# Optimization experiments

Measured on AMD Instinct MI355X. Metric: run time of the kernel, lower is better.

Reference implementation:

```python
import jax, jax.numpy as jnp
import numpy as np

EMO = 1024
FEAT = 1024
K = 128  # aggregation_k
H_LIST = (4, 8, 16)
D_LIST = tuple(EMO // h for h in H_LIST)  # (256, 128, 64)
D_SUM = sum(D_LIST)  # 448
H_SUM = sum(H_LIST)  # 28
N = len(H_LIST)      # 3 subspaces
TEMP = float(np.power(D_SUM, 0.5))


def _block_mask(sizes, total):
    m = np.zeros((len(sizes), total), np.float32)
    off = 0
    for i, s in enumerate(sizes):
        m[i, off:off + s] = 1.0
        off += s
    return jnp.asarray(m)

M_Q_BLK = _block_mask(D_LIST, D_SUM)  # [N, d_sum]
M_V_BLK = _block_mask(H_LIST, H_SUM)  # [N, h_sum]


def setup_inputs() -> dict:
    key = jax.random.key(0)
    ks = iter(jax.random.split(key, 32))
    nrm = lambda shape, s=1.0: jax.random.normal(next(ks), shape, jnp.float32) * s
    B, Lt, Lp, Nv = 32, 1024, 512, 256
    return {
        "emo_embedding": nrm((B, Lt, EMO)),
        "phr_feat": nrm((B, Lp, FEAT)),
        "video_feat": nrm((B, Nv, FEAT)),
        "w_v_W": nrm((FEAT, FEAT), FEAT ** -0.5), "w_v_b": nrm((FEAT,), 0.01),
        "agg_a_W": nrm((FEAT, K), FEAT ** -0.5), "agg_a_b": nrm((K,), 0.01),
        "agg_c_W": nrm((FEAT, EMO), FEAT ** -0.5), "agg_c_b": nrm((EMO,), 0.01),
        "ele_W": nrm((2 * EMO, 1), (2 * EMO) ** -0.5), "ele_b": nrm((1,), 0.01),
        "wq_W": nrm((EMO, D_SUM), EMO ** -0.5), "wq_b": nrm((D_SUM,), 0.01),
        "wk_W": nrm((EMO, D_SUM), EMO ** -0.5), "wk_b": nrm((D_SUM,), 0.01),
        "wv_W": nrm((EMO, H_SUM), EMO ** -0.5), "wv_b": nrm((H_SUM,), 0.01),
        "wr_W": nrm((EMO, N), EMO ** -0.5), "wr_b": nrm((N,), 0.01),
    }


def reference(emo_embedding, phr_feat, video_feat,
              w_v_W, w_v_b, agg_a_W, agg_a_b, agg_c_W, agg_c_b,
              ele_W, ele_b, wq_W, wq_b, wk_W, wk_b, wv_W, wv_b, wr_W, wr_b):
    B, Lt, _ = emo_embedding.shape
    Nv = video_feat.shape[1]
    Lp = phr_feat.shape[1]

    # --- feature_aggregation ---
    # AdaptiveAvgPool1d(Nv); Lp % Nv == 0 so it is an exact reshape-mean.
    phr = phr_feat.reshape(B, Nv, Lp // Nv, FEAT).mean(axis=2)
    combine = jnp.concatenate([phr @ w_v_W + w_v_b, video_feat], axis=1)   # [B, 2*Nv, FEAT]
    attn_a = jax.nn.softmax(combine @ agg_a_W + agg_a_b, axis=-1)          # [B, 2*Nv, K]
    agg_feat = jnp.einsum('bmk,bme->bke', attn_a, combine @ agg_c_W + agg_c_b)  # [B, K, EMO]

    # --- element_routing ---
    A_pool = jnp.einsum('ble,bke->blk', emo_embedding, agg_feat).mean(axis=1)   # [B, K]
    route = jnp.einsum('bk,bke->be', A_pool, agg_feat)[:, None, :]              # [B, 1, EMO]
    route = jnp.broadcast_to(route, emo_embedding.shape)
    R_e = jnp.tanh(jnp.concatenate([emo_embedding, route], axis=-1) @ ele_W + ele_b)  # [B, Lt, 1]
    route_emo = R_e * emo_embedding                                              # [B, Lt, EMO]

    # --- subspace_routing ---
    Q = route_emo @ wq_W + wq_b        # [B, Lt, d_sum]
    Kp = agg_feat @ wk_W + wk_b        # [B, K, d_sum]
    V = agg_feat @ wv_W + wv_b         # [B, K, h_sum]
    Rp = agg_feat @ wr_W + wr_b        # [B, K, N]

    # N masked copies of Q (block subspace masks); K/R are plain repeats, V is masked.
    Qm = (Q[:, None] * M_Q_BLK[None, :, None, :]).reshape(B, N * Lt, D_SUM)
    Kf = jnp.tile(Kp, (1, N, 1))                                         # [B, N*K, d_sum]
    Vf = (V[:, None] * M_V_BLK[None, :, None, :]).reshape(B, N * K, H_SUM)
    Rf = jnp.tile(Rp, (1, N, 1))                                         # [B, N*K, N]

    attn = jax.nn.softmax(jnp.einsum('bqd,bkd->bqk', Qm, Kf) / TEMP, axis=-1)  # [B, N*Lt, N*K]
    O = jnp.tanh(attn @ Vf).reshape(B, N, Lt, H_SUM)
    O_R = (attn @ Rf).reshape(B, N, Lt, N)

    # per-subspace head gating of route_emo
    T_list = []
    hoff = 0
    for i in range(N):
        hi, di = H_LIST[i], D_LIST[i]
        ori = route_emo.reshape(B, Lt, hi, di)
        Oi = O[:, i, :, hoff:hoff + hi][..., None]      # [B, Lt, hi, 1]
        T_list.append((ori * Oi).reshape(B, Lt, EMO))
        hoff += hi
    T = jnp.stack(T_list, axis=1)                        # [B, N, Lt, EMO]

    Rdiag = jnp.stack([O_R[:, j, :, j].mean(axis=-1) for j in range(N)], axis=1)  # [B, N]
    gate = jax.nn.softmax(Rdiag, axis=-1)[:, :, None, None]
    return emo_embedding + (gate * T).sum(axis=1)
```

## Files before the change

### kernel.cpp

```cpp
#include <hip/hip_runtime.h>
#include <math.h>

typedef long long i64;
typedef __attribute__((ext_vector_type(8))) short bf16x8;
typedef __attribute__((ext_vector_type(4))) float f32x4;

#define TEMP_ISQ 0.047245559f

__device__ __forceinline__ unsigned short f2b(float x) {
  union { float f; unsigned u; } a; a.f = x;
  return (unsigned short)((a.u + 0x7fffu + ((a.u >> 16) & 1u)) >> 16);
}
__device__ __forceinline__ float b2f(unsigned short b) {
  union { float f; unsigned u; } a; a.u = ((unsigned)b) << 16; return a.f;
}

template<int BIAS, int OUTM, int RS, int BZDIV, int XMODE = 0>
__global__ __launch_bounds__(256)
void gemm_mfma(const unsigned short* __restrict__ Ab, i64 sA,
               const unsigned short* __restrict__ Bb, i64 sB,
               const float* __restrict__ bias,
               void* __restrict__ Ob, i64 sO,
               unsigned short* __restrict__ O2b, i64 sO2,
               int Nn, int Kd, int ldA, int ldB, int ldO,
               const float* __restrict__ rowScale, i64 sRS,
               const float* __restrict__ rsAdd)
{
  __shared__ unsigned short As[2][4096];
  __shared__ unsigned short Bs[2][4096];
  const int tid = threadIdx.x;
  const int w = tid >> 6, lane = tid & 63;

  const int gx = gridDim.x, gy = gridDim.y;
  int nwg = gx * gy * gridDim.z;
  int bid = blockIdx.x + gx * (blockIdx.y + gy * blockIdx.z);
  int L = bid;
  if ((nwg & 7) == 0) L = (bid & 7) * (nwg >> 3) + (bid >> 3);
  const int bx = L % gx;
  int rem = L / gx;
  const int by = rem % gy;
  const int z  = rem / gy;

  const int m0 = by * 128, n0 = bx * 128;
  const unsigned short* A;
  const unsigned short* B;
  int KdL = Kd;
  if (XMODE == 1) {
    int bb = z / 3, ii = z - bb * 3;
    const int dof_[3] = {0, 256, 384};
    const int kdt_[3] = {256, 128, 64};
    A = Ab + dof_[ii] + (i64)bb * sA;
    B = Bb + dof_[ii] + (i64)bb * sB;
    KdL = kdt_[ii];
  } else {
    A = Ab + (i64)z * sA;
    B = Bb + (i64)(BZDIV == 1 ? z : z / BZDIV) * sB;
  }
  const int wr = w >> 1, wc = w & 1;
  const int rS = tid >> 2, sS = tid & 3;
  const int cL = lane & 15, sl = lane >> 4;

  f32x4 acc[4][4];
  #pragma unroll
  for (int i = 0; i < 4; ++i)
    #pragma unroll
    for (int j = 0; j < 4; ++j) acc[i][j] = (f32x4){0.f, 0.f, 0.f, 0.f};

  auto STAGE = [&](int buf, int k0) {
    #pragma unroll
    for (int q = 0; q < 2; ++q) {
      int r = rS + q * 64;
      int sg = sS ^ (r & 3);
      const unsigned short* sa = A + (i64)(m0 + r) * ldA + k0 + sg * 8;
      const unsigned short* sb = B + (i64)(n0 + r) * ldB + k0 + sg * 8;
      __builtin_amdgcn_global_load_lds(
          (__attribute__((address_space(1))) void*)sa,
          (__attribute__((address_space(3))) void*)&As[buf][r * 32 + sS * 8], 16, 0, 0);
      __builtin_amdgcn_global_load_lds(
          (__attribute__((address_space(1))) void*)sb,
          (__attribute__((address_space(3))) void*)&Bs[buf][r * 32 + sS * 8], 16, 0, 0);
    }
  };

  STAGE(0, 0);
  __syncthreads();

  for (int k0 = 0; k0 < KdL; k0 += 32) {
    const int cur = (k0 >> 5) & 1;
    if (k0 + 32 < KdL) STAGE(cur ^ 1, k0 + 32);
    bf16x8 af[4], bfv[4];
    #pragma unroll
    for (int mi = 0; mi < 4; ++mi) {
      int rr = wr * 64 + mi * 16 + cL;
      int ph = sl ^ (rr & 3);
      af[mi] = *(const bf16x8*)&As[cur][rr * 32 + ph * 8];
    }
    #pragma unroll
    for (int ni = 0; ni < 4; ++ni) {
      int rr = wc * 64 + ni * 16 + cL;
      int ph = sl ^ (rr & 3);
      bfv[ni] = *(const bf16x8*)&Bs[cur][rr * 32 + ph * 8];
    }
    #pragma unroll
    for (int mi = 0; mi < 4; ++mi)
      #pragma unroll
      for (int ni = 0; ni < 4; ++ni)
        acc[mi][ni] = __builtin_amdgcn_mfma_f32_16x16x32_bf16(af[mi], bfv[ni], acc[mi][ni], 0, 0, 0);
    __syncthreads();
  }

  #pragma unroll
  for (int mi = 0; mi < 4; ++mi) {
    const int rowb = m0 + wr * 64 + mi * 16 + sl * 4;
    #pragma unroll
    for (int ni = 0; ni < 4; ++ni) {
      const int col = n0 + wc * 64 + ni * 16 + cL;
      if (col < Nn) {
        float bc = (BIAS == 1) ? bias[col] : 0.f;
        #pragma unroll
        for (int rg = 0; rg < 4; ++rg) {
          float v = acc[mi][ni][rg];
          if (RS) v *= tanhf(rowScale[(i64)z * sRS + rowb + rg] + rsAdd[z]);
          v += bc;
          if (BIAS == 2) v += bias[rowb + rg];
          i64 oidx = (i64)(rowb + rg) * ldO + col;
          if (OUTM == 0)      ((float*)Ob)[(i64)z * sO + oidx] = v;
          else if (OUTM == 1) ((unsigned short*)Ob)[(i64)z * sO + oidx] = f2b(v);
          else if (OUTM == 3) ((float*)Ob)[(i64)z * sO + oidx] = tanhf(v * (1.f / 3.f));
          else {
            ((float*)Ob)[(i64)z * sO + oidx] = v;
            O2b[(i64)z * sO2 + oidx] = f2b(v);
          }
        }
      }
    }
  }
}

__global__ __launch_bounds__(256)
void emo_pass1(const float* __restrict__ emo, const float* __restrict__ eleW,
               unsigned short* __restrict__ emoB, float* __restrict__ colPart,
               float* __restrict__ dotE) {
  int b = blockIdx.y, lc = blockIdx.x;
  int t = threadIdx.x, lane = t & 63, w = t >> 6;
  float4 w4 = ((const float4*)eleW)[t];
  float4 acc = make_float4(0.f, 0.f, 0.f, 0.f);
  __shared__ float dw[16][4];
  const float4* src = (const float4*)emo + ((i64)b * 1024 + lc * 16) * 256;
  ushort4* dst = (ushort4*)emoB + ((i64)b * 1024 + lc * 16) * 256;
  #pragma unroll 4
  for (int lr = 0; lr < 16; ++lr) {
    float4 v = src[lr * 256 + t];
    acc.x += v.x; acc.y += v.y; acc.z += v.z; acc.w += v.w;
    float d = v.x * w4.x + v.y * w4.y + v.z * w4.z + v.w * w4.w;
    #pragma unroll
    for (int o = 32; o; o >>= 1) d += __shfl_xor(d, o);
    if (!lane) dw[lr][w] = d;
    ushort4 o4; o4.x = f2b(v.x); o4.y = f2b(v.y); o4.z = f2b(v.z); o4.w = f2b(v.w);
    dst[lr * 256 + t] = o4;
  }
  __syncthreads();
  if (t < 16) dotE[(i64)b * 1024 + lc * 16 + t] = dw[t][0] + dw[t][1] + dw[t][2] + dw[t][3];
  ((float4*)colPart)[((i64)b * 64 + lc) * 256 + t] = acc;
}

__global__ void colmean2(const float* __restrict__ colPart, float* __restrict__ emomean) {
  int b = blockIdx.y, e = blockIdx.x * 256 + threadIdx.x;
  float s = 0.f;
  #pragma unroll 8
  for (int lc = 0; lc < 64; ++lc) s += colPart[((i64)b * 64 + lc) * 1024 + e];
  emomean[b * 1024 + e] = s * (1.f / 1024.f);
}

__global__ __launch_bounds__(256)
void transpose_all(const float* __restrict__ w_v_W, const float* __restrict__ agg_a_W,
                   const float* __restrict__ agg_c_W, const float* __restrict__ wq_W,
                   const float* __restrict__ wk_W, const float* __restrict__ wv_W,
                   const float* __restrict__ wr_W,
                   unsigned short* __restrict__ wvT, unsigned short* __restrict__ aaT,
                   unsigned short* __restrict__ acT, unsigned short* __restrict__ wqT,
                   unsigned short* __restrict__ kvrT) {
  __shared__ float T[32][33];
  int bx = blockIdx.x;
  const float* in; unsigned short* out; int N, Npad, s0;
  if (bx < 32)      { in = w_v_W;   out = wvT;                     N = 1024; Npad = 1024; s0 = 0; }
  else if (bx < 36) { in = agg_a_W; out = aaT;                     N = 128;  Npad = 128;  s0 = 32; }
  else if (bx < 68) { in = agg_c_W; out = acT;                     N = 1024; Npad = 1024; s0 = 36; }
  else if (bx < 84) { in = wq_W;    out = wqT;                     N = 448;  Npad = 512;  s0 = 68; }
  else if (bx < 98) { in = wk_W;    out = kvrT;                    N = 448;  Npad = 448;  s0 = 84; }
  else if (bx < 99) { in = wv_W;    out = kvrT + (i64)448 * 1024;  N = 28;   Npad = 28;   s0 = 98; }
  else              { in = wr_W;    out = kvrT + (i64)476 * 1024;  N = 3;    Npad = 36;   s0 = 99; }
  int n0 = (bx - s0) * 32, k0 = blockIdx.y * 32;
  int t = threadIdx.x;
  #pragma unroll
  for (int p = 0; p < 4; ++p) {
    int idx = t + 256 * p; int kk = idx >> 5, nn = idx & 31;
    float v = 0.f;
    if (n0 + nn < N) v = in[(i64)(k0 + kk) * N + (n0 + nn)];
    T[nn][kk] = v;
  }
  __syncthreads();
  #pragma unroll
  for (int p = 0; p < 4; ++p) {
    int idx = t + 256 * p; int nn = idx >> 5, kk = idx & 31;
    if (n0 + nn < Npad) out[(i64)(n0 + nn) * 1024 + (k0 + kk)] = f2b(T[nn][kk]);
  }
}

__global__ void kvr_bias_kernel(const float* wkb, const float* wvb, const float* wrb, float* out) {
  int t = blockIdx.x * 256 + threadIdx.x;
  if (t >= 480) return;
  out[t] = (t < 448) ? wkb[t] : (t < 476) ? wvb[t - 448] : (t < 479) ? wrb[t - 476] : 0.f;
}

__global__ void pool_phr(const float* __restrict__ phr, unsigned short* __restrict__ out) {
  i64 idx = (i64)blockIdx.x * 256 + threadIdx.x;
  if (idx >= 2097152) return;
  i64 bm = idx >> 8; int c = (int)(idx & 255);
  i64 b = bm >> 8, m = bm & 255;
  const float4* r0 = (const float4*)(phr + (b * 512 + 2 * m) * 1024) + c;
  const float4* r1 = (const float4*)(phr + (b * 512 + 2 * m + 1) * 1024) + c;
  float4 a = *r0, d = *r1;
  ushort4 o;
  o.x = f2b(0.5f * (a.x + d.x)); o.y = f2b(0.5f * (a.y + d.y));
  o.z = f2b(0.5f * (a.z + d.z)); o.w = f2b(0.5f * (a.w + d.w));
  ((ushort4*)out)[idx] = o;
}

__global__ void vconv(const float* __restrict__ video, unsigned short* __restrict__ combine) {
  i64 idx = (i64)blockIdx.x * 256 + threadIdx.x;
  if (idx >= 2097152) return;
  i64 b = idx >> 16, r = idx & 65535;
  float4 v = ((const float4*)video)[idx];
  ushort4 o;
  o.x = f2b(v.x); o.y = f2b(v.y); o.z = f2b(v.z); o.w = f2b(v.w);
  ((ushort4*)combine)[b * 131072 + 65536 + r] = o;
}

__global__ void vt_fill(const unsigned short* __restrict__ KVR, unsigned short* __restrict__ VT) {
  int b = blockIdx.y;
  int idx = blockIdx.x * 256 + threadIdx.x;
  int n = idx >> 7, k = idx & 127;
  unsigned short v = 0;
  if (n < 28) v = KVR[(i64)b * 61440 + k * 480 + 448 + n];
  VT[((i64)b * 128 + n) * 128 + k] = v;
}

__global__ void softmax_attn_a(const float* __restrict__ logits, unsigned short* __restrict__ outT) {
  int gw = (int)(((i64)blockIdx.x * blockDim.x + threadIdx.x) >> 6);
  int lane = threadIdx.x & 63;
  if (gw >= 32 * 512) return;
  int b = gw >> 9, m = gw & 511;
  const float* p = logits + (i64)gw * 128;
  float x0 = p[lane], x1 = p[lane + 64];
  float mx = fmaxf(x0, x1);
  #pragma unroll
  for (int o = 32; o; o >>= 1) mx = fmaxf(mx, __shfl_xor(mx, o));
  float e0 = expf(x0 - mx), e1 = expf(x1 - mx);
  float s = e0 + e1;
  #pragma unroll
  for (int o = 32; o; o >>= 1) s += __shfl_xor(s, o);
  float inv = 1.f / s;
  unsigned short* o0 = outT + (i64)b * 128 * 512 + m;
  o0[(i64)lane * 512] = f2b(e0 * inv);
  o0[(i64)(lane + 64) * 512] = f2b(e1 * inv);
}

__global__ void softmax_P_bf(const unsigned short* __restrict__ PL, unsigned short* __restrict__ P) {
  i64 gw = ((i64)blockIdx.x * blockDim.x + threadIdx.x) >> 6;
  int lane = threadIdx.x & 63;
  if (gw >= 98304) return;
  const unsigned short* p = PL + gw * 128;
  float x0 = b2f(p[lane]) * TEMP_ISQ, x1 = b2f(p[lane + 64]) * TEMP_ISQ;
  float mx = fmaxf(x0, x1);
  #pragma unroll
  for (int o = 32; o; o >>= 1) mx = fmaxf(mx, __shfl_xor(mx, o));
  float e0 = expf(x0 - mx), e1 = expf(x1 - mx);
  float s = e0 + e1;
  #pragma unroll
  for (int o = 32; o; o >>= 1) s += __shfl_xor(s, o);
  float inv = 1.f / s;
  P[gw * 128 + lane] = f2b(e0 * inv);
  P[gw * 128 + lane + 64] = f2b(e1 * inv);
}

__global__ void apool_kernel(const float* __restrict__ emomean, const float* __restrict__ agg,
                             float* __restrict__ Apool) {
  int gw = (int)(((i64)blockIdx.x * blockDim.x + threadIdx.x) >> 6);
  int lane = threadIdx.x & 63;
  if (gw >= 32 * 128) return;
  int b = gw >> 7, k = gw & 127;
  const float* ag = agg + ((i64)b * 128 + k) * 1024;
  const float* em = emomean + (i64)b * 1024;
  float s = 0.f;
  #pragma unroll
  for (int j = 0; j < 16; ++j) { int e = j * 64 + lane; s += em[e] * ag[e]; }
  #pragma unroll
  for (int o = 32; o; o >>= 1) s += __shfl_down(s, o);
  if (!lane) Apool[gw] = s;
}

__global__ void route_kernel(const float* __restrict__ Apool, const float* __restrict__ agg,
                             float* __restrict__ route) {
  int b = blockIdx.y;
  int e = blockIdx.x * 256 + threadIdx.x;
  __shared__ float Ap[128];
  if (threadIdx.x < 128) Ap[threadIdx.x] = Apool[b * 128 + threadIdx.x];
  __syncthreads();
  const float* ag = agg + (i64)b * 128 * 1024 + e;
  float s = 0.f;
  #pragma unroll 8
  for (int k = 0; k < 128; ++k) s += Ap[k] * ag[(i64)k * 1024];
  route[b * 1024 + e] = s;
}

__global__ void rb_kernel(const float* __restrict__ route, const float* __restrict__ eleW,
                          const float* __restrict__ eleb, float* __restrict__ rb) {
  int b = blockIdx.x, t = threadIdx.x;
  float s = 0.f;
  for (int j = t; j < 1024; j += 256) s += route[b * 1024 + j] * eleW[1024 + j];
  __shared__ float red[256];
  red[t] = s; __syncthreads();
  for (int o = 128; o > 0; o >>= 1) { if (t < o) red[t] += red[t + o]; __syncthreads(); }
  if (t == 0) rb[b] = red[0] + eleb[0];
}

__global__ void pmean1_kernel(const unsigned short* __restrict__ P, float* __restrict__ Ppart) {
  int bi = blockIdx.x, c = blockIdx.y, k = threadIdx.x;
  const unsigned short* p = P + ((i64)bi * 1024 + c * 128) * 128 + k;
  float s = 0.f;
  for (int l = 0; l < 128; ++l) s += b2f(p[(i64)l * 128]);
  Ppart[((i64)bi * 8 + c) * 128 + k] = s;
}

__global__ void pmean2_rdiag(const float* __restrict__ Ppart, const unsigned short* __restrict__ KVR,
                             float* __restrict__ gate) {
  int b = blockIdx.x, t = threadIdx.x;
  __shared__ float red[128];
  __shared__ float rd[3];
  for (int i = 0; i < 3; ++i) {
    float s = 0.f;
    #pragma unroll
    for (int c = 0; c < 8; ++c) s += Ppart[((i64)(b * 3 + i) * 8 + c) * 128 + t];
    float v = s * (1.f / 1024.f) * b2f(KVR[(i64)b * 61440 + t * 480 + 476 + i]);
    red[t] = v; __syncthreads();
    for (int o = 64; o > 0; o >>= 1) { if (t < o) red[t] += red[t + o]; __syncthreads(); }
    if (t == 0) rd[i] = red[0];
    __syncthreads();
  }
  if (t == 0) {
    float m = fmaxf(rd[0], fmaxf(rd[1], rd[2]));
    float e0 = expf(rd[0] - m), e1 = expf(rd[1] - m), e2 = expf(rd[2] - m);
    float inv = 1.f / (e0 + e1 + e2);
    gate[b * 3 + 0] = e0 * inv; gate[b * 3 + 1] = e1 * inv; gate[b * 3 + 2] = e2 * inv;
  }
}

__global__ __launch_bounds__(256)
void final_kernel(const unsigned short* __restrict__ emoB, const float* __restrict__ dotE,
                  const float* __restrict__ rbv, const float* __restrict__ O,
                  const float* __restrict__ gate, float* __restrict__ out) {
  i64 bl = blockIdx.x;
  int b = (int)(bl >> 10), l = (int)(bl & 1023);
  __shared__ float Gg[16];
  int t = threadIdx.x;
  if (t < 16) {
    float g0 = gate[b * 3], g1 = gate[b * 3 + 1], g2 = gate[b * 3 + 2];
    float o0 = O[((i64)(b * 3 + 0) * 1024 + l) * 28 + (t >> 2)];
    float o1 = O[((i64)(b * 3 + 1) * 1024 + l) * 28 + 4 + (t >> 1)];
    float o2 = O[((i64)(b * 3 + 2) * 1024 + l) * 28 + 12 + t];
    Gg[t] = g0 * o0 + g1 * o1 + g2 * o2;
  }
  __syncthreads();
  float re = tanhf(dotE[bl] + rbv[b]);
  ushort4 e4 = ((const ushort4*)(emoB + bl * 1024))[t];
  float g = 1.f + re * Gg[t >> 4];
  ((float4*)(out + bl * 1024))[t] =
      make_float4(b2f(e4.x) * g, b2f(e4.y) * g, b2f(e4.z) * g, b2f(e4.w) * g);
}

extern "C" void kernel_launch(void* const* d_in, const int* in_sizes, int n_in,
                              void* d_out, int out_size, void* d_ws, size_t ws_size,
                              hipStream_t stream) {
  const float* emo     = (const float*)d_in[0];
  const float* phr     = (const float*)d_in[1];
  const float* video   = (const float*)d_in[2];
  const float* w_v_W   = (const float*)d_in[3];
  const float* w_v_b   = (const float*)d_in[4];
  const float* agg_a_W = (const float*)d_in[5];
  const float* agg_a_b = (const float*)d_in[6];
  const float* agg_c_W = (const float*)d_in[7];
  const float* agg_c_b = (const float*)d_in[8];
  const float* ele_W   = (const float*)d_in[9];
  const float* ele_b   = (const float*)d_in[10];
  const float* wq_W    = (const float*)d_in[11];
  const float* wq_b    = (const float*)d_in[12];
  const float* wk_W    = (const float*)d_in[13];
  const float* wk_b    = (const float*)d_in[14];
  const float* wv_W    = (const float*)d_in[15];
  const float* wv_b    = (const float*)d_in[16];
  const float* wr_W    = (const float*)d_in[17];
  const float* wr_b    = (const float*)d_in[18];

  char* ws = (char*)d_ws;
  const i64 oEmoB    = 0;
  const i64 oCombine = 67108864;
  const i64 oPL      = 67108864;
  const i64 oPooled  = 100663296;
  const i64 oLogitsA = 100663296;
  const i64 oAggF    = 100663296;
  const i64 oO       = 100663296;
  const i64 oCT      = 117440512;
  const i64 oQ       = 117440512;
  const i64 oAttnAT  = 150994944;
  const i64 oAggB    = 155189248;
  const i64 oWvT     = 163577856;
  const i64 oAaT     = 165675008;
  const i64 oAcT     = 165937152;
  const i64 oWqT     = 168034304;
  const i64 oKvrT    = 169082880;
  const i64 oKVR     = 170131456;
  const i64 oVT      = 174063616;
  const i64 oKvrB    = 175112192;
  const i64 oEmomean = 175116288;
  const i64 oColPart = 175247360;
  const i64 oDotE    = 183635968;
  const i64 oApool   = 183767040;
  const i64 oRoute   = 183783424;
  const i64 oRb      = 183914496;
  const i64 oPpart   = 183914752;
  const i64 oGate    = 184307968;

  unsigned short* emoB    = (unsigned short*)(ws + oEmoB);
  unsigned short* combine = (unsigned short*)(ws + oCombine);
  unsigned short* PL      = (unsigned short*)(ws + oPL);
  unsigned short* P       = PL;
  unsigned short* pooled  = (unsigned short*)(ws + oPooled);
  float*          logitsA = (float*)(ws + oLogitsA);
  float*          aggF    = (float*)(ws + oAggF);
  float*          O       = (float*)(ws + oO);
  unsigned short* CT      = (unsigned short*)(ws + oCT);
  unsigned short* Q       = (unsigned short*)(ws + oQ);
  unsigned short* attnAT  = (unsigned short*)(ws + oAttnAT);
  unsigned short* aggB    = (unsigned short*)(ws + oAggB);
  unsigned short* wvT     = (unsigned short*)(ws + oWvT);
  unsigned short* aaT     = (unsigned short*)(ws + oAaT);
  unsigned short* acT     = (unsigned short*)(ws + oAcT);
  unsigned short* wqT     = (unsigned short*)(ws + oWqT);
  unsigned short* kvrT    = (unsigned short*)(ws + oKvrT);
  unsigned short* KVR     = (unsigned short*)(ws + oKVR);
  unsigned short* VT      = (unsigned short*)(ws + oVT);
  float*          kvrB    = (float*)(ws + oKvrB);
  float*          emomean = (float*)(ws + oEmomean);
  float*          colPart = (float*)(ws + oColPart);
  float*          dotE    = (float*)(ws + oDotE);
  float*          Apool   = (float*)(ws + oApool);
  float*          route   = (float*)(ws + oRoute);
  float*          rbv     = (float*)(ws + oRb);
  float*          Ppart   = (float*)(ws + oPpart);
  float*          gate    = (float*)(ws + oGate);

  dim3 blk(256);

  emo_pass1<<<dim3(64, 32), blk, 0, stream>>>(emo, ele_W, emoB, colPart, dotE);

  transpose_all<<<dim3(101, 32), blk, 0, stream>>>(w_v_W, agg_a_W, agg_c_W, wq_W, wk_W, wv_W, wr_W,
                                                   wvT, aaT, acT, wqT, kvrT);
  kvr_bias_kernel<<<2, blk, 0, stream>>>(wk_b, wv_b, wr_b, kvrB);

  pool_phr<<<8192, blk, 0, stream>>>(phr, pooled);
  vconv<<<8192, blk, 0, stream>>>(video, combine);
  gemm_mfma<1, 1, 0, 1><<<dim3(8, 2, 32), blk, 0, stream>>>(pooled, 262144, wvT, 0, w_v_b,
      (void*)combine, 524288, nullptr, 0, 1024, 1024, 1024, 1024, 1024, nullptr, 0, nullptr);
  gemm_mfma<1, 0, 0, 1><<<dim3(1, 4, 32), blk, 0, stream>>>(combine, 524288, aaT, 0, agg_a_b,
      (void*)logitsA, 65536, nullptr, 0, 128, 1024, 1024, 1024, 128, nullptr, 0, nullptr);
  softmax_attn_a<<<4096, blk, 0, stream>>>(logitsA, attnAT);
  gemm_mfma<2, 1, 0, 1><<<dim3(4, 8, 32), blk, 0, stream>>>(acT, 0, combine, 524288, agg_c_b,
      (void*)CT, 524288, nullptr, 0, 512, 1024, 1024, 1024, 512, nullptr, 0, nullptr);
  gemm_mfma<0, 2, 0, 1><<<dim3(8, 1, 32), blk, 0, stream>>>(attnAT, 65536, CT, 524288, nullptr,
      (void*)aggF, 131072, aggB, 131072, 1024, 512, 512, 512, 1024, nullptr, 0, nullptr);

  colmean2<<<dim3(4, 32), blk, 0, stream>>>(colPart, emomean);
  apool_kernel<<<1024, blk, 0, stream>>>(emomean, aggF, Apool);
  route_kernel<<<dim3(4, 32), blk, 0, stream>>>(Apool, aggF, route);
  rb_kernel<<<32, blk, 0, stream>>>(route, ele_W, ele_b, rbv);

  gemm_mfma<1, 1, 0, 1><<<dim3(4, 1, 32), blk, 0, stream>>>(aggB, 131072, kvrT, 0, kvrB,
      (void*)KVR, 61440, nullptr, 0, 480, 1024, 1024, 1024, 480, nullptr, 0, nullptr);
  vt_fill<<<dim3(64, 32), blk, 0, stream>>>(KVR, VT);
  gemm_mfma<1, 1, 1, 1><<<dim3(4, 8, 32), blk, 0, stream>>>(emoB, 1048576, wqT, 0, wq_b,
      (void*)Q, 458752, nullptr, 0, 448, 1024, 1024, 1024, 448, dotE, 1024, rbv);

  gemm_mfma<0, 1, 0, 1, 1><<<dim3(1, 8, 96), blk, 0, stream>>>(Q, 458752, KVR, 61440, nullptr,
      (void*)PL, 131072, nullptr, 0, 128, 0, 448, 480, 128, nullptr, 0, nullptr);

  softmax_P_bf<<<24576, blk, 0, stream>>>(PL, P);
  pmean1_kernel<<<dim3(96, 8), 128, 0, stream>>>(P, Ppart);
  gemm_mfma<0, 3, 0, 3><<<dim3(1, 8, 96), blk, 0, stream>>>(P, 131072, VT, 16384, nullptr,
      (void*)O, 28672, nullptr, 0, 28, 128, 128, 128, 28, nullptr, 0, nullptr);
  pmean2_rdiag<<<32, 128, 0, stream>>>(Ppart, KVR, gate);
  final_kernel<<<32768, blk, 0, stream>>>(emoB, dotE, rbv, O, gate, (float*)d_out);
}
```

Measured before the change: 460.4 us.

## Reassociate Q·K by folding the key projection into per-subspace query weights

Instead of projecting emo into Q and then multiplying Q by K per subspace, each batch and subspace first forms a 128x1024 fused weight from the K slice times the matching wq slice. The attention logits then come from a single GEMM of emoB against that fused weight, with a precomputed per-key bias from K·wq_b. This removes the Q intermediate, its round trip through memory and one GEMM stage, but adds a small extra GEMM, a bias kernel and an extra bf16 rounding of the fused weights. The LDS XOR swizzle is also changed to use bits 1-2 of the row index, aimed at reducing bank conflicts in every MFMA GEMM.

New measurement: 453.9 us. About the same (-1.4%).

```diff
diff --git a/kernel.cpp b/kernel.cpp
--- a/kernel.cpp
+++ b/kernel.cpp
@@ -42,16 +42,20 @@
   const int z  = rem / gy;
 
   const int m0 = by * 128, n0 = bx * 128;
+  int zA = (XMODE == 2) ? z / 3 : z;
   const unsigned short* A;
   const unsigned short* B;
   int KdL = Kd;
-  if (XMODE == 1) {
+  if (XMODE == 3) {
     int bb = z / 3, ii = z - bb * 3;
     const int dof_[3] = {0, 256, 384};
     const int kdt_[3] = {256, 128, 64};
-    A = Ab + dof_[ii] + (i64)bb * sA;
-    B = Bb + dof_[ii] + (i64)bb * sB;
+    A = Ab + (i64)bb * sA + dof_[ii];
+    B = Bb + dof_[ii];
     KdL = kdt_[ii];
+  } else if (XMODE == 2) {
+    A = Ab + (i64)zA * sA;
+    B = Bb + (i64)z * sB;
   } else {
     A = Ab + (i64)z * sA;
     B = Bb + (i64)(BZDIV == 1 ? z : z / BZDIV) * sB;
@@ -70,7 +74,7 @@
     #pragma unroll
     for (int q = 0; q < 2; ++q) {
       int r = rS + q * 64;
-      int sg = sS ^ (r & 3);
+      int sg = sS ^ ((r >> 1) & 3);
       const unsigned short* sa = A + (i64)(m0 + r) * ldA + k0 + sg * 8;
       const unsigned short* sb = B + (i64)(n0 + r) * ldB + k0 + sg * 8;
       __builtin_amdgcn_global_load_lds(
@@ -92,13 +96,13 @@
     #pragma unroll
     for (int mi = 0; mi < 4; ++mi) {
       int rr = wr * 64 + mi * 16 + cL;
-      int ph = sl ^ (rr & 3);
+      int ph = sl ^ ((rr >> 1) & 3);
       af[mi] = *(const bf16x8*)&As[cur][rr * 32 + ph * 8];
     }
     #pragma unroll
     for (int ni = 0; ni < 4; ++ni) {
       int rr = wc * 64 + ni * 16 + cL;
-      int ph = sl ^ (rr & 3);
+      int ph = sl ^ ((rr >> 1) & 3);
       bfv[ni] = *(const bf16x8*)&Bs[cur][rr * 32 + ph * 8];
     }
     #pragma unroll
@@ -109,6 +113,7 @@
     __syncthreads();
   }
 
+  const float* bp = (XMODE == 2) ? (bias + (i64)z * 128) : bias;
   #pragma unroll
   for (int mi = 0; mi < 4; ++mi) {
     const int rowb = m0 + wr * 64 + mi * 16 + sl * 4;
@@ -116,11 +121,11 @@
     for (int ni = 0; ni < 4; ++ni) {
       const int col = n0 + wc * 64 + ni * 16 + cL;
       if (col < Nn) {
-        float bc = (BIAS == 1) ? bias[col] : 0.f;
+        float bc = (BIAS == 1) ? bp[col] : 0.f;
         #pragma unroll
         for (int rg = 0; rg < 4; ++rg) {
           float v = acc[mi][ni][rg];
-          if (RS) v *= tanhf(rowScale[(i64)z * sRS + rowb + rg] + rsAdd[z]);
+          if (RS) v *= tanhf(rowScale[(i64)zA * sRS + rowb + rg] + rsAdd[zA]);
           v += bc;
           if (BIAS == 2) v += bias[rowb + rg];
           i64 oidx = (i64)(rowb + rg) * ldO + col;
@@ -178,20 +183,26 @@
                    const float* __restrict__ wk_W, const float* __restrict__ wv_W,
                    const float* __restrict__ wr_W,
                    unsigned short* __restrict__ wvT, unsigned short* __restrict__ aaT,
-                   unsigned short* __restrict__ acT, unsigned short* __restrict__ wqT,
+                   unsigned short* __restrict__ acT, unsigned short* __restrict__ wqB,
                    unsigned short* __restrict__ kvrT) {
+  int bx = blockIdx.x;
+  int t = threadIdx.x;
+  if (bx >= 84) {
+    i64 li = (((i64)(bx - 84) * 32 + blockIdx.y) * 256 + t) * 4;
+    float4 v = *(const float4*)(wq_W + li);
+    ushort4 o; o.x = f2b(v.x); o.y = f2b(v.y); o.z = f2b(v.z); o.w = f2b(v.w);
+    *(ushort4*)(wqB + li) = o;
+    return;
+  }
   __shared__ float T[32][33];
-  int bx = blockIdx.x;
   const float* in; unsigned short* out; int N, Npad, s0;
   if (bx < 32)      { in = w_v_W;   out = wvT;                     N = 1024; Npad = 1024; s0 = 0; }
   else if (bx < 36) { in = agg_a_W; out = aaT;                     N = 128;  Npad = 128;  s0 = 32; }
   else if (bx < 68) { in = agg_c_W; out = acT;                     N = 1024; Npad = 1024; s0 = 36; }
-  else if (bx < 84) { in = wq_W;    out = wqT;                     N = 448;  Npad = 512;  s0 = 68; }
-  else if (bx < 98) { in = wk_W;    out = kvrT;                    N = 448;  Npad = 448;  s0 = 84; }
-  else if (bx < 99) { in = wv_W;    out = kvrT + (i64)448 * 1024;  N = 28;   Npad = 28;   s0 = 98; }
-  else              { in = wr_W;    out = kvrT + (i64)476 * 1024;  N = 3;    Npad = 36;   s0 = 99; }
+  else if (bx < 82) { in = wk_W;    out = kvrT;                    N = 448;  Npad = 448;  s0 = 68; }
+  else if (bx < 83) { in = wv_W;    out = kvrT + (i64)448 * 1024;  N = 28;   Npad = 28;   s0 = 82; }
+  else              { in = wr_W;    out = kvrT + (i64)476 * 1024;  N = 3;    Npad = 36;   s0 = 83; }
   int n0 = (bx - s0) * 32, k0 = blockIdx.y * 32;
-  int t = threadIdx.x;
   #pragma unroll
   for (int p = 0; p < 4; ++p) {
     int idx = t + 256 * p; int kk = idx >> 5, nn = idx & 31;
@@ -211,6 +222,20 @@
   int t = blockIdx.x * 256 + threadIdx.x;
   if (t >= 480) return;
   out[t] = (t < 448) ? wkb[t] : (t < 476) ? wvb[t - 448] : (t < 479) ? wrb[t - 476] : 0.f;
+}
+
+__global__ void qb_kernel(const unsigned short* __restrict__ KVR, const float* __restrict__ wq_b,
+                          float* __restrict__ qb) {
+  int zz = blockIdx.x;
+  int bb = zz / 3, ii = zz - bb * 3;
+  const int dof_[3] = {0, 256, 384};
+  const int kdt_[3] = {256, 128, 64};
+  int k = threadIdx.x;
+  const unsigned short* kp = KVR + (i64)bb * 61440 + k * 480 + dof_[ii];
+  const float* wb = wq_b + dof_[ii];
+  float s = 0.f;
+  for (int d = 0; d < kdt_[ii]; ++d) s += b2f(kp[d]) * wb[d];
+  qb[zz * 128 + k] = s;
 }
 
 __global__ void pool_phr(const float* __restrict__ phr, unsigned short* __restrict__ out) {
@@ -411,13 +436,13 @@
   const i64 oAggF    = 100663296;
   const i64 oO       = 100663296;
   const i64 oCT      = 117440512;
-  const i64 oQ       = 117440512;
+  const i64 oW2T     = 117440512;
   const i64 oAttnAT  = 150994944;
   const i64 oAggB    = 155189248;
   const i64 oWvT     = 163577856;
   const i64 oAaT     = 165675008;
   const i64 oAcT     = 165937152;
-  const i64 oWqT     = 168034304;
+  const i64 oWqB     = 168034304;
   const i64 oKvrT    = 169082880;
   const i64 oKVR     = 170131456;
   const i64 oVT      = 174063616;
@@ -440,13 +465,13 @@
   float*          aggF    = (float*)(ws + oAggF);
   float*          O       = (float*)(ws + oO);
   unsigned short* CT      = (unsigned short*)(ws + oCT);
-  unsigned short* Q       = (unsigned short*)(ws + oQ);
+  unsigned short* W2T     = (unsigned short*)(ws + oW2T);
   unsigned short* attnAT  = (unsigned short*)(ws + oAttnAT);
   unsigned short* aggB    = (unsigned short*)(ws + oAggB);
   unsigned short* wvT     = (unsigned short*)(ws + oWvT);
   unsigned short* aaT     = (unsigned short*)(ws + oAaT);
   unsigned short* acT     = (unsigned short*)(ws + oAcT);
-  unsigned short* wqT     = (unsigned short*)(ws + oWqT);
+  unsigned short* wqB     = (unsigned short*)(ws + oWqB);
   unsigned short* kvrT    = (unsigned short*)(ws + oKvrT);
   unsigned short* KVR     = (unsigned short*)(ws + oKVR);
   unsigned short* VT      = (unsigned short*)(ws + oVT);
@@ -456,6 +481,7 @@
   float*          dotE    = (float*)(ws + oDotE);
   float*          Apool   = (float*)(ws + oApool);
   float*          route   = (float*)(ws + oRoute);
+  float*          qb      = (float*)(ws + oRoute);
   float*          rbv     = (float*)(ws + oRb);
   float*          Ppart   = (float*)(ws + oPpart);
   float*          gate    = (float*)(ws + oGate);
@@ -464,8 +490,8 @@
 
   emo_pass1<<<dim3(64, 32), blk, 0, stream>>>(emo, ele_W, emoB, colPart, dotE);
 
-  transpose_all<<<dim3(101, 32), blk, 0, stream>>>(w_v_W, agg_a_W, agg_c_W, wq_W, wk_W, wv_W, wr_W,
-                                                   wvT, aaT, acT, wqT, kvrT);
+  transpose_all<<<dim3(98, 32), blk, 0, stream>>>(w_v_W, agg_a_W, agg_c_W, wq_W, wk_W, wv_W, wr_W,
+                                                  wvT, aaT, acT, wqB, kvrT);
   kvr_bias_kernel<<<2, blk, 0, stream>>>(wk_b, wv_b, wr_b, kvrB);
 
   pool_phr<<<8192, blk, 0, stream>>>(phr, pooled);
@@ -488,11 +514,13 @@
   gemm_mfma<1, 1, 0, 1><<<dim3(4, 1, 32), blk, 0, stream>>>(aggB, 131072, kvrT, 0, kvrB,
       (void*)KVR, 61440, nullptr, 0, 480, 1024, 1024, 1024, 480, nullptr, 0, nullptr);
   vt_fill<<<dim3(64, 32), blk, 0, stream>>>(KVR, VT);
-  gemm_mfma<1, 1, 1, 1><<<dim3(4, 8, 32), blk, 0, stream>>>(emoB, 1048576, wqT, 0, wq_b,
-      (void*)Q, 458752, nullptr, 0, 448, 1024, 1024, 1024, 448, dotE, 1024, rbv);
-
-  gemm_mfma<0, 1, 0, 1, 1><<<dim3(1, 8, 96), blk, 0, stream>>>(Q, 458752, KVR, 61440, nullptr,
-      (void*)PL, 131072, nullptr, 0, 128, 0, 448, 480, 128, nullptr, 0, nullptr);
+
+  gemm_mfma<0, 1, 0, 1, 3><<<dim3(8, 1, 96), blk, 0, stream>>>(KVR, 61440, wqB, 0, nullptr,
+      (void*)W2T, 131072, nullptr, 0, 1024, 0, 480, 448, 1024, nullptr, 0, nullptr);
+  qb_kernel<<<96, 128, 0, stream>>>(KVR, wq_b, qb);
+
+  gemm_mfma<1, 1, 1, 1, 2><<<dim3(1, 8, 96), blk, 0, stream>>>(emoB, 1048576, W2T, 131072, qb,
+      (void*)PL, 131072, nullptr, 0, 128, 1024, 1024, 1024, 128, dotE, 1024, rbv);
 
   softmax_P_bf<<<24576, blk, 0, stream>>>(PL, P);
   pmean1_kernel<<<dim3(96, 8), 128, 0, stream>>>(P, Ppart);
```
